# Kernel tuning notes

Measured on AMD Instinct MI355X. Metric: run time of the kernel, lower is better.

Reference implementation:

```python
import jax, jax.numpy as jnp
from jax import lax
import numpy as np

B, H, W = 4, 512, 512
CIN, COUT, BASE, NL = 3, 3, 64, 4
EPS = 1e-5


def _conv(x, w, b, stride=1, pad=0):
    y = lax.conv_general_dilated(x, w, (stride, stride), ((pad, pad), (pad, pad)),
                                 dimension_numbers=('NCHW', 'OIHW', 'NCHW'))
    return y + b[None, :, None, None]


def _convT(x, w, b):
    # torch ConvTranspose2d(k=3, stride=2, padding=1, output_padding=1); w is [Cin, Cout, 3, 3]
    w_ = jnp.flip(w, (2, 3)).transpose(1, 0, 2, 3)  # -> OIHW
    k = w.shape[2]
    lo, hi = k - 1 - 1, k - 1 - 1 + 1  # (1, 2): pad=1, output_padding=1
    y = lax.conv_general_dilated(x, w_, (1, 1), ((lo, hi), (lo, hi)), lhs_dilation=(2, 2),
                                 dimension_numbers=('NCHW', 'OIHW', 'NCHW'))
    return y + b[None, :, None, None]


def _inorm(x):
    m = x.mean((2, 3), keepdims=True)
    v = x.var((2, 3), keepdims=True)  # biased, matches torch InstanceNorm2d
    return (x - m) * lax.rsqrt(v + EPS)


def _refl(x, p=3):
    return jnp.pad(x, ((0, 0), (0, 0), (p, p), (p, p)), mode='reflect')


def setup_inputs() -> dict:
    key = jax.random.key(0)
    ks = jax.random.split(key, 16)
    s = 0.05
    inp = {}
    inp['x'] = jax.random.normal(ks[0], (B, CIN, H, W), jnp.float32)
    inp['inst'] = jax.random.randint(ks[1], (B, 1, H, W), 0, 10)
    inp['w0'] = jax.random.normal(ks[2], (BASE, CIN, 7, 7), jnp.float32) * s
    inp['b0'] = jnp.zeros((BASE,), jnp.float32)
    c, ki = BASE, 3
    for i in range(NL):
        inp[f'dw{i}'] = jax.random.normal(ks[ki], (2 * c, c, 3, 3), jnp.float32) * s
        inp[f'db{i}'] = jnp.zeros((2 * c,), jnp.float32)
        c *= 2; ki += 1
    for i in range(NL):
        inp[f'uw{i}'] = jax.random.normal(ks[ki], (c, c // 2, 3, 3), jnp.float32) * s  # torch ConvT layout [Cin,Cout,k,k]
        inp[f'ub{i}'] = jnp.zeros((c // 2,), jnp.float32)
        c //= 2; ki += 1
    inp['wf'] = jax.random.normal(ks[ki], (COUT, BASE, 7, 7), jnp.float32) * s
    inp['bf'] = jnp.zeros((COUT,), jnp.float32)
    return inp


def reference(x, w0, b0, dw0, db0, dw1, db1, dw2, db2, dw3, db3,
              uw0, ub0, uw1, ub1, uw2, ub2, uw3, ub3, wf, bf, inst):
    h = jax.nn.relu(_inorm(_conv(_refl(x), w0, b0)))
    for w_, b_ in ((dw0, db0), (dw1, db1), (dw2, db2), (dw3, db3)):
        h = jax.nn.relu(_inorm(_conv(h, w_, b_, stride=2, pad=1)))
    for w_, b_ in ((uw0, ub0), (uw1, ub1), (uw2, ub2), (uw3, ub3)):
        h = jax.nn.relu(_inorm(_convT(h, w_, b_)))
    h = jnp.tanh(_conv(_refl(h), wf, bf))
    # instancewise_average_pooling: original loops classes but always masks inst==1,
    # so the result is the per-(batch, channel) mean over inst==1 pixels scattered
    # back onto those pixels, zeros elsewhere.
    mask = (inst == 1).astype(h.dtype)            # [B,1,H,W]
    cnt = mask.sum((2, 3))                        # [B,1]
    mean = (h * mask).sum((2, 3)) / cnt           # [B,C]
    return mean[:, :, None, None] * mask
```

## Files before the change

kernel.cpp:

```cpp
#include <hip/hip_runtime.h>
#include <math.h>


typedef _Float16 half_t;
typedef _Float16 halfx8 __attribute__((ext_vector_type(8)));
typedef _Float16 halfx4 __attribute__((ext_vector_type(4)));
typedef float floatx4 __attribute__((ext_vector_type(4)));

static __device__ __forceinline__ float xform(float v, float m, float r) {
  v = (v - m) * r;
  return v > 0.f ? v : 0.f;
}

__global__ __launch_bounds__(256) void transform_w(
    const float* __restrict__ src, half_t* __restrict__ dst,
    int Cin, int Cout, int mode)
{
  int idx = blockIdx.x * 256 + threadIdx.x;
  int total = Cin * Cout * 9;
  if (idx >= total) return;
  int tap = idx % 9, t2 = idx / 9;
  int co, ci;
  if (mode == 0) { ci = t2 % Cin; co = t2 / Cin; }
  else           { co = t2 % Cout; ci = t2 / Cout; }
  dst[((size_t)tap * Cout + co) * Cin + ci] = (half_t)src[idx];
}

__global__ __launch_bounds__(256) void transform_wf(
    const float* __restrict__ src, half_t* __restrict__ dst)
{
  int idx = blockIdx.x * 256 + threadIdx.x;
  if (idx >= 49 * 16 * 64) return;
  int ci = idx & 63, t = idx >> 6;
  int co = t & 15, tap = t >> 4;
  float v = (co < 3) ? src[((size_t)co * 64 + ci) * 49 + tap] : 0.f;
  dst[idx] = (half_t)v;
}

__global__ __launch_bounds__(256) void conv0_kernel(
    const float* __restrict__ x, const float* __restrict__ w,
    const float* __restrict__ bias, half_t* __restrict__ out)
{
  const int H = 512, W = 512, CIN = 3;
  __shared__ float s_in[3][22][22];
  __shared__ float4 s_w[3 * 49][4];
  const int cog = blockIdx.x, tile = blockIdx.y, b = blockIdx.z;
  const int tx0 = (tile & 31) << 4, ty0 = (tile >> 5) << 4;
  const int tid = threadIdx.x, tx = tid & 15, ty = tid >> 4;

  for (int idx = tid; idx < CIN * 49 * 16; idx += 256) {
    int j = idx & 15, r = idx >> 4;
    ((float*)s_w)[r * 16 + j] = w[(cog * 16 + j) * (CIN * 49) + r];
  }
  for (int idx = tid; idx < CIN * 22 * 22; idx += 256) {
    int ci = idx / 484, rr = idx % 484;
    int iy = rr / 22, ix = rr % 22;
    int gy = ty0 + iy - 3, gx = tx0 + ix - 3;
    gy = gy < 0 ? -gy : (gy >= H ? 2 * H - 2 - gy : gy);
    gx = gx < 0 ? -gx : (gx >= W ? 2 * W - 2 - gx : gx);
    s_in[ci][iy][ix] = x[((size_t)(b * CIN + ci) * H + gy) * W + gx];
  }
  __syncthreads();

  float acc[16];
#pragma unroll
  for (int j = 0; j < 16; ++j) acc[j] = 0.f;

#pragma unroll
  for (int ci = 0; ci < 3; ++ci)
    for (int ky = 0; ky < 7; ++ky)
#pragma unroll
      for (int kx = 0; kx < 7; ++kx) {
        float v = s_in[ci][ty + ky][tx + kx];
        int r = (ci * 7 + ky) * 7 + kx;
#pragma unroll
        for (int q = 0; q < 4; ++q) {
          float4 wv = s_w[r][q];
          acc[q * 4 + 0] += v * wv.x;
          acc[q * 4 + 1] += v * wv.y;
          acc[q * 4 + 2] += v * wv.z;
          acc[q * 4 + 3] += v * wv.w;
        }
      }
  const int oy = ty0 + ty, ox = tx0 + tx;
  halfx8 o0, o1;
#pragma unroll
  for (int j = 0; j < 8; ++j) {
    o0[j] = (half_t)(acc[j] + bias[cog * 16 + j]);
    o1[j] = (half_t)(acc[8 + j] + bias[cog * 16 + 8 + j]);
  }
  size_t obase = ((size_t)(b * 512 + oy) * 512 + ox) * 64 + cog * 16;
  *(halfx8*)(&out[obase]) = o0;
  *(halfx8*)(&out[obase + 8]) = o1;
}

__global__ __launch_bounds__(256) void stats_part(
    const half_t* __restrict__ x, float* __restrict__ Ssum, int C, int S)
{
  const int b = blockIdx.y, tid = threadIdx.x;
  const size_t base = (size_t)b * S * C;
  const int E8 = (S * C) >> 3;
  float s[8], s2[8];
#pragma unroll
  for (int j = 0; j < 8; ++j) { s[j] = 0.f; s2[j] = 0.f; }
  for (int i8 = blockIdx.x * 256 + tid; i8 < E8; i8 += gridDim.x * 256) {
    halfx8 v = *(const halfx8*)(x + base + (size_t)i8 * 8);
#pragma unroll
    for (int j = 0; j < 8; ++j) {
      float f = (float)v[j];
      s[j] += f; s2[j] += f * f;
    }
  }
  __shared__ float part[256][16];
#pragma unroll
  for (int j = 0; j < 8; ++j) { part[tid][j] = s[j]; part[tid][8 + j] = s2[j]; }
  __syncthreads();
  const int T = C >> 3, reps = 256 / (C >> 3);
  for (int c = tid; c < C; c += 256) {
    int r = c >> 3, j = c & 7;
    float ss = 0.f, ss2 = 0.f;
    for (int m = 0; m < reps; ++m) {
      ss += part[r + m * T][j];
      ss2 += part[r + m * T][8 + j];
    }
    atomicAdd(&Ssum[(size_t)(b * C + c) * 2], ss);
    atomicAdd(&Ssum[(size_t)(b * C + c) * 2 + 1], ss2);
  }
}

__global__ __launch_bounds__(256) void finalize_stats(
    const float* __restrict__ Ssum, float* __restrict__ mean,
    float* __restrict__ rstd, int total, float invN)
{
  int idx = blockIdx.x * 256 + threadIdx.x;
  if (idx >= total) return;
  float sm = Ssum[(size_t)idx * 2], s2 = Ssum[(size_t)idx * 2 + 1];
  float m = sm * invN;
  float var = s2 * invN - m * m;
  mean[idx] = m;
  rstd[idx] = rsqrtf(var + 1e-5f);
}

__global__ __launch_bounds__(256) void down_mfma(
    const half_t* __restrict__ in, const half_t* __restrict__ wt,
    const float* __restrict__ bias, const float* __restrict__ mean,
    const float* __restrict__ rstd, half_t* __restrict__ out,
    int Cin, int Cout, int IH, int IW)
{
  const int OH = IH >> 1, OW = IW >> 1;
  __shared__ _Float16 sX[9 * 33 * 40];
  const int tid = threadIdx.x;
  const int wave = tid >> 6, lane = tid & 63;
  const int ln = lane & 15, g = lane >> 4;
  const int cog = blockIdx.x, b = blockIdx.z;
  const int ntx = OW >> 4;
  const int ox0 = (blockIdx.y % ntx) << 4, oy0 = (blockIdx.y / ntx) << 2;
  const int iy0 = 2 * oy0 - 1, ix0 = 2 * ox0 - 1;
  const int coW = cog * 128 + wave * 32;
  const int q = tid & 3;

  floatx4 acc[4][2];
#pragma unroll
  for (int r = 0; r < 4; ++r)
#pragma unroll
    for (int n = 0; n < 2; ++n) acc[r][n] = floatx4{0.f, 0.f, 0.f, 0.f};

  for (int c0 = 0; c0 < Cin; c0 += 32) {
    float mq[8], rq[8];
#pragma unroll
    for (int j = 0; j < 8; ++j) {
      int cc = c0 + q * 8 + j;
      mq[j] = mean[b * Cin + cc];
      rq[j] = rstd[b * Cin + cc];
    }
    __syncthreads();
    for (int idx = tid; idx < 9 * 33 * 4; idx += 256) {
      int p = idx >> 2;
      int y = p / 33, xx = p % 33;
      int gy = iy0 + y, gx = ix0 + xx;
      halfx8 v = {0, 0, 0, 0, 0, 0, 0, 0};
      if ((unsigned)gy < (unsigned)IH && (unsigned)gx < (unsigned)IW) {
        v = *(const halfx8*)(in + ((size_t)(b * IH + gy) * IW + gx) * Cin + c0 + q * 8);
#pragma unroll
        for (int j = 0; j < 8; ++j) {
          float f = ((float)v[j] - mq[j]) * rq[j];
          v[j] = (_Float16)(f > 0.f ? f : 0.f);
        }
      }
      *(halfx8*)(&sX[(y * 33 + xx) * 40 + q * 8]) = v;
    }
    __syncthreads();
#pragma unroll
    for (int tap = 0; tap < 9; ++tap) {
      const int ky = tap / 3, kx = tap % 3;
      halfx8 wb0 = *(const halfx8*)(wt + ((size_t)tap * Cout + coW + ln) * Cin + c0 + g * 8);
      halfx8 wb1 = *(const halfx8*)(wt + ((size_t)tap * Cout + coW + 16 + ln) * Cin + c0 + g * 8);
#pragma unroll
      for (int r = 0; r < 4; ++r) {
        halfx8 a = *(const halfx8*)(&sX[((2 * r + ky) * 33 + 2 * ln + kx) * 40 + g * 8]);
        acc[r][0] = __builtin_amdgcn_mfma_f32_16x16x32_f16(a, wb0, acc[r][0], 0, 0, 0);
        acc[r][1] = __builtin_amdgcn_mfma_f32_16x16x32_f16(a, wb1, acc[r][1], 0, 0, 0);
      }
    }
  }
#pragma unroll
  for (int nt = 0; nt < 2; ++nt) {
    int co = coW + nt * 16 + ln;
    float bs = bias[co];
#pragma unroll
    for (int r = 0; r < 4; ++r)
#pragma unroll
      for (int i = 0; i < 4; ++i) {
        int oy = oy0 + r, ox = ox0 + g * 4 + i;
        out[((size_t)(b * OH + oy) * OW + ox) * Cout + co] = (half_t)(acc[r][nt][i] + bs);
      }
  }
}

__global__ __launch_bounds__(256) void up_mfma(
    const half_t* __restrict__ in, const half_t* __restrict__ wt,
    const float* __restrict__ bias, const float* __restrict__ mean,
    const float* __restrict__ rstd, half_t* __restrict__ out,
    int Cin, int Cout, int IH, int IW)
{
  const int OH = IH << 1, OW = IW << 1;
  __shared__ _Float16 sX[5 * 17 * 40];
  const int tid = threadIdx.x;
  const int wave = tid >> 6, lane = tid & 63;
  const int ln = lane & 15, g = lane >> 4;
  const int cog = blockIdx.x, b = blockIdx.z;
  const int ntx = OW >> 5;
  const int ox0 = (blockIdx.y % ntx) << 5, oy0 = (blockIdx.y / ntx) << 3;
  const int iyb = oy0 >> 1, ixb = ox0 >> 1;
  const int co = cog * 64 + wave * 16 + ln;
  const int q = tid & 3;

  floatx4 acc[4][4];
#pragma unroll
  for (int c = 0; c < 4; ++c)
#pragma unroll
    for (int r = 0; r < 4; ++r) acc[c][r] = floatx4{0.f, 0.f, 0.f, 0.f};

  for (int c0 = 0; c0 < Cin; c0 += 32) {
    float mq[8], rq[8];
#pragma unroll
    for (int j = 0; j < 8; ++j) {
      int cc = c0 + q * 8 + j;
      mq[j] = mean[b * Cin + cc];
      rq[j] = rstd[b * Cin + cc];
    }
    __syncthreads();
    for (int idx = tid; idx < 5 * 17 * 4; idx += 256) {
      int p = idx >> 2;
      int y = p / 17, xx = p % 17;
      int gy = iyb + y, gx = ixb + xx;
      halfx8 v = {0, 0, 0, 0, 0, 0, 0, 0};
      if (gy < IH && gx < IW) {
        v = *(const halfx8*)(in + ((size_t)(b * IH + gy) * IW + gx) * Cin + c0 + q * 8);
#pragma unroll
        for (int j = 0; j < 8; ++j) {
          float f = ((float)v[j] - mq[j]) * rq[j];
          v[j] = (_Float16)(f > 0.f ? f : 0.f);
        }
      }
      *(halfx8*)(&sX[(y * 17 + xx) * 40 + q * 8]) = v;
    }
    __syncthreads();
#pragma unroll
    for (int tap = 0; tap < 9; ++tap) {
      const int ky = tap / 3, kx = tap % 3;
      const int cls = ((ky == 1) ? 0 : 2) + ((kx == 1) ? 0 : 1);
      const int dy = (ky == 0) ? 1 : 0;
      const int dx = (kx == 0) ? 1 : 0;
      halfx8 wb = *(const halfx8*)(wt + ((size_t)tap * Cout + co) * Cin + c0 + g * 8);
#pragma unroll
      for (int r = 0; r < 4; ++r) {
        halfx8 a = *(const halfx8*)(&sX[((r + dy) * 17 + ln + dx) * 40 + g * 8]);
        acc[cls][r] = __builtin_amdgcn_mfma_f32_16x16x32_f16(a, wb, acc[cls][r], 0, 0, 0);
      }
    }
  }
  float bs = bias[co];
#pragma unroll
  for (int cls = 0; cls < 4; ++cls) {
    const int ey = cls >> 1, ex = cls & 1;
#pragma unroll
    for (int r = 0; r < 4; ++r)
#pragma unroll
      for (int i = 0; i < 4; ++i) {
        int oy = oy0 + 2 * r + ey;
        int ox = ox0 + 2 * (g * 4 + i) + ex;
        out[((size_t)(b * OH + oy) * OW + ox) * Cout + co] = (half_t)(acc[cls][r][i] + bs);
      }
  }
}

__global__ __launch_bounds__(256) void convf_mfma(
    const half_t* __restrict__ in, const half_t* __restrict__ wt,
    const float* __restrict__ bias, const float* __restrict__ mean,
    const float* __restrict__ rstd, float* __restrict__ out)
{
  const int H = 512, W = 512;
  __shared__ _Float16 sX[22 * 22 * 72];
  const int tile = blockIdx.x, b = blockIdx.y;
  const int tx0 = (tile & 31) << 4, ty0 = (tile >> 5) << 4;
  const int tid = threadIdx.x;
  const int wave = tid >> 6, lane = tid & 63;
  const int ln = lane & 15, g = lane >> 4;
  const int oct = tid & 7;

  float mq[8], rq[8];
#pragma unroll
  for (int j = 0; j < 8; ++j) {
    mq[j] = mean[b * 64 + oct * 8 + j];
    rq[j] = rstd[b * 64 + oct * 8 + j];
  }
  for (int u = tid; u < 484 * 8; u += 256) {
    int p = u >> 3;
    int iy = p / 22, ix = p % 22;
    int gy = ty0 + iy - 3, gx = tx0 + ix - 3;
    gy = gy < 0 ? -gy : (gy >= H ? 2 * H - 2 - gy : gy);
    gx = gx < 0 ? -gx : (gx >= W ? 2 * W - 2 - gx : gx);
    halfx8 v = *(const halfx8*)(in + ((size_t)(b * H + gy) * W + gx) * 64 + oct * 8);
#pragma unroll
    for (int j = 0; j < 8; ++j) {
      float f = ((float)v[j] - mq[j]) * rq[j];
      v[j] = (_Float16)(f > 0.f ? f : 0.f);
    }
    *(halfx8*)(&sX[p * 72 + oct * 8]) = v;
  }
  __syncthreads();

  floatx4 acc[4];
#pragma unroll
  for (int r = 0; r < 4; ++r) acc[r] = floatx4{0.f, 0.f, 0.f, 0.f};

  for (int tap = 0; tap < 49; ++tap) {
    const int ky = tap / 7, kx = tap % 7;
#pragma unroll
    for (int kc = 0; kc < 2; ++kc) {
      halfx8 wb = *(const halfx8*)(wt + ((size_t)tap * 16 + ln) * 64 + kc * 32 + g * 8);
#pragma unroll
      for (int rr = 0; rr < 4; ++rr) {
        int y = wave * 4 + rr;
        halfx8 a = *(const halfx8*)(&sX[((y + ky) * 22 + ln + kx) * 72 + kc * 32 + g * 8]);
        acc[rr] = __builtin_amdgcn_mfma_f32_16x16x32_f16(a, wb, acc[rr], 0, 0, 0);
      }
    }
  }
  if (ln < 3) {
    float bs = bias[ln];
#pragma unroll
    for (int rr = 0; rr < 4; ++rr) {
      int oy = ty0 + wave * 4 + rr;
#pragma unroll
      for (int i = 0; i < 4; ++i) {
        int ox = tx0 + g * 4 + i;
        out[((size_t)(b * 3 + ln) * H + oy) * W + ox] = tanhf(acc[rr][i] + bs);
      }
    }
  }
}

__global__ __launch_bounds__(256) void pool_sum_kernel(
    const float* __restrict__ f, const int* __restrict__ inst,
    float* __restrict__ P)
{
  const int N = 512 * 512;
  const int b = blockIdx.x, chunk = blockIdx.y;
  const int per = N / 32;
  const int base = chunk * per;
  float s0 = 0.f, s1 = 0.f, s2 = 0.f, c = 0.f;
  for (int i = base + threadIdx.x; i < base + per; i += 256) {
    if (inst[b * N + i] == 1) {
      c += 1.f;
      s0 += f[(size_t)(b * 3 + 0) * N + i];
      s1 += f[(size_t)(b * 3 + 1) * N + i];
      s2 += f[(size_t)(b * 3 + 2) * N + i];
    }
  }
#pragma unroll
  for (int off = 32; off > 0; off >>= 1) {
    s0 += __shfl_down(s0, off); s1 += __shfl_down(s1, off);
    s2 += __shfl_down(s2, off); c += __shfl_down(c, off);
  }
  __shared__ float red[4][4];
  int wv = threadIdx.x >> 6;
  if ((threadIdx.x & 63) == 0) {
    red[wv][0] = s0; red[wv][1] = s1; red[wv][2] = s2; red[wv][3] = c;
  }
  __syncthreads();
  if (threadIdx.x == 0) {
    float t0 = red[0][0] + red[1][0] + red[2][0] + red[3][0];
    float t1 = red[0][1] + red[1][1] + red[2][1] + red[3][1];
    float t2 = red[0][2] + red[1][2] + red[2][2] + red[3][2];
    float tc = red[0][3] + red[1][3] + red[2][3] + red[3][3];
    atomicAdd(&P[b * 4 + 0], t0);
    atomicAdd(&P[b * 4 + 1], t1);
    atomicAdd(&P[b * 4 + 2], t2);
    atomicAdd(&P[b * 4 + 3], tc);
  }
}

__global__ __launch_bounds__(256) void pool_scatter_kernel(
    const int* __restrict__ inst, const float* __restrict__ P,
    float* __restrict__ out)
{
  const int N = 512 * 512;
  int idx = blockIdx.x * 256 + threadIdx.x;
  if (idx >= 4 * N) return;
  int b = idx >> 18;
  int i = idx & (N - 1);
  bool m = inst[idx] == 1;
  float inv = 1.f / P[b * 4 + 3];
  out[(size_t)(b * 3 + 0) * N + i] = m ? P[b * 4 + 0] * inv : 0.f;
  out[(size_t)(b * 3 + 1) * N + i] = m ? P[b * 4 + 1] * inv : 0.f;
  out[(size_t)(b * 3 + 2) * N + i] = m ? P[b * 4 + 2] * inv : 0.f;
}

extern "C" void kernel_launch(void* const* d_in, const int* in_sizes, int n_in,
                              void* d_out, int out_size, void* d_ws, size_t ws_size,
                              hipStream_t stream)
{
  (void)in_sizes; (void)n_in; (void)out_size; (void)ws_size;
  const float* x    = (const float*)d_in[0];
  const int*   inst = (const int*)d_in[1];
  const float* w0   = (const float*)d_in[2];
  const float* b0   = (const float*)d_in[3];
  const float *dw[4], *db[4], *uw[4], *ub[4];
  for (int i = 0; i < 4; ++i) {
    dw[i] = (const float*)d_in[4 + 2 * i];
    db[i] = (const float*)d_in[5 + 2 * i];
    uw[i] = (const float*)d_in[12 + 2 * i];
    ub[i] = (const float*)d_in[13 + 2 * i];
  }
  const float* wf = (const float*)d_in[20];
  const float* bf = (const float*)d_in[21];

  char* base = (char*)d_ws;
  half_t* A  = (half_t*)base;
  half_t* Bh = (half_t*)(base + 134217728);
  float*  F  = (float*)(base + 134217728);
  float*  Ssum   = (float*)(base + 201326592);
  float*  S_mean = (float*)(base + 201326592 + 32768);
  float*  S_rstd = (float*)(base + 201326592 + 49152);
  float*  P      = (float*)(base + 201326592 + 65536);
  half_t* WTp0   = (half_t*)(base + 201326592 + 66560);
  half_t* WTp1   = (half_t*)(base + 201326592 + 66560 + 147456);
  half_t* WTf    = (half_t*)(base + 201326592 + 66560 + 294912);
  half_t* WTA    = (half_t*)(base + 124780544);
  half_t* WTB    = (half_t*)(base + 191889408);

  auto XFORM = [&](const float* src, half_t* dst, int Ci, int Co, int mode) {
    int tot = Ci * Co * 9;
    transform_w<<<dim3((tot + 255) / 256), 256, 0, stream>>>(src, dst, Ci, Co, mode);
  };
  auto STATS = [&](const half_t* p, int C, int S) {
    hipMemsetAsync(Ssum, 0, 4096 * 2 * sizeof(float), stream);
    stats_part<<<dim3(128, 4), 256, 0, stream>>>(p, Ssum, C, S);
    finalize_stats<<<dim3((4 * C + 255) / 256), 256, 0, stream>>>(
        Ssum, S_mean, S_rstd, 4 * C, 1.f / (float)S);
  };

  conv0_kernel<<<dim3(4, 1024, 4), 256, 0, stream>>>(x, w0, b0, A);
  transform_wf<<<dim3((49 * 16 * 64 + 255) / 256), 256, 0, stream>>>(wf, WTf);
  STATS(A, 64, 512 * 512);

  XFORM(dw[0], WTp0, 64, 128, 0);
  down_mfma<<<dim3(1, 1024, 4), 256, 0, stream>>>(A, WTp0, db[0], S_mean, S_rstd, Bh, 64, 128, 512, 512);
  STATS(Bh, 128, 256 * 256);
  XFORM(dw[1], WTA, 128, 256, 0);
  down_mfma<<<dim3(2, 256, 4), 256, 0, stream>>>(Bh, WTA, db[1], S_mean, S_rstd, A, 128, 256, 256, 256);
  STATS(A, 256, 128 * 128);
  XFORM(dw[2], WTB, 256, 512, 0);
  down_mfma<<<dim3(4, 64, 4), 256, 0, stream>>>(A, WTB, db[2], S_mean, S_rstd, Bh, 256, 512, 128, 128);
  STATS(Bh, 512, 64 * 64);
  XFORM(dw[3], WTA, 512, 1024, 0);
  down_mfma<<<dim3(8, 16, 4), 256, 0, stream>>>(Bh, WTA, db[3], S_mean, S_rstd, A, 512, 1024, 64, 64);
  STATS(A, 1024, 32 * 32);

  XFORM(uw[0], WTB, 1024, 512, 1);
  up_mfma<<<dim3(8, 16, 4), 256, 0, stream>>>(A, WTB, ub[0], S_mean, S_rstd, Bh, 1024, 512, 32, 32);
  STATS(Bh, 512, 64 * 64);
  XFORM(uw[1], WTA, 512, 256, 1);
  up_mfma<<<dim3(4, 64, 4), 256, 0, stream>>>(Bh, WTA, ub[1], S_mean, S_rstd, A, 512, 256, 64, 64);
  STATS(A, 256, 128 * 128);
  XFORM(uw[2], WTA, 256, 128, 1);
  up_mfma<<<dim3(2, 256, 4), 256, 0, stream>>>(A, WTA, ub[2], S_mean, S_rstd, Bh, 256, 128, 128, 128);
  STATS(Bh, 128, 256 * 256);
  XFORM(uw[3], WTp1, 128, 64, 1);
  up_mfma<<<dim3(1, 1024, 4), 256, 0, stream>>>(Bh, WTp1, ub[3], S_mean, S_rstd, A, 128, 64, 256, 256);
  STATS(A, 64, 512 * 512);

  convf_mfma<<<dim3(1024, 4), 256, 0, stream>>>(A, WTf, bf, S_mean, S_rstd, F);
  hipMemsetAsync(P, 0, 16 * sizeof(float), stream);
  pool_sum_kernel<<<dim3(4, 32), 256, 0, stream>>>(F, inst, P);
  pool_scatter_kernel<<<dim3(4096), 256, 0, stream>>>(inst, P, (float*)d_out);
}
```

Baseline: 1.856 ms.

## Rewrite 7x7 stem convolution as fp16 MFMA implicit GEMM

```diff
diff --git a/kernel.cpp b/kernel.cpp
--- a/kernel.cpp
+++ b/kernel.cpp
@@ -37,61 +37,90 @@
   dst[idx] = (half_t)v;
 }
 
-__global__ __launch_bounds__(256) void conv0_kernel(
-    const float* __restrict__ x, const float* __restrict__ w,
+__global__ __launch_bounds__(256) void transform_w0(
+    const float* __restrict__ src, half_t* __restrict__ dst)
+{
+  int idx = blockIdx.x * 256 + threadIdx.x;
+  if (idx >= 7 * 64 * 32) return;
+  int k = idx & 31, t = idx >> 5;
+  int co = t & 63, ky = t >> 6;
+  int kx = k >> 2, ci = k & 3;
+  float v = (ci < 3 && kx < 7) ? src[(((size_t)co * 3 + ci) * 7 + ky) * 7 + kx] : 0.f;
+  dst[idx] = (half_t)v;
+}
+
+__global__ __launch_bounds__(256) void conv0_mfma(
+    const float* __restrict__ x, const half_t* __restrict__ wt,
     const float* __restrict__ bias, half_t* __restrict__ out)
 {
-  const int H = 512, W = 512, CIN = 3;
-  __shared__ float s_in[3][22][22];
-  __shared__ float4 s_w[3 * 49][4];
-  const int cog = blockIdx.x, tile = blockIdx.y, b = blockIdx.z;
+  const int H = 512, W = 512;
+  __shared__ _Float16 sX[22 * 24 * 4];
+  __shared__ _Float16 sO[256 * 72];
+  const int tile = blockIdx.x, b = blockIdx.y;
   const int tx0 = (tile & 31) << 4, ty0 = (tile >> 5) << 4;
-  const int tid = threadIdx.x, tx = tid & 15, ty = tid >> 4;
-
-  for (int idx = tid; idx < CIN * 49 * 16; idx += 256) {
-    int j = idx & 15, r = idx >> 4;
-    ((float*)s_w)[r * 16 + j] = w[(cog * 16 + j) * (CIN * 49) + r];
-  }
-  for (int idx = tid; idx < CIN * 22 * 22; idx += 256) {
-    int ci = idx / 484, rr = idx % 484;
-    int iy = rr / 22, ix = rr % 22;
-    int gy = ty0 + iy - 3, gx = tx0 + ix - 3;
-    gy = gy < 0 ? -gy : (gy >= H ? 2 * H - 2 - gy : gy);
-    gx = gx < 0 ? -gx : (gx >= W ? 2 * W - 2 - gx : gx);
-    s_in[ci][iy][ix] = x[((size_t)(b * CIN + ci) * H + gy) * W + gx];
+  const int tid = threadIdx.x;
+  const int wave = tid >> 6, lane = tid & 63;
+  const int ln = lane & 15, g = lane >> 4;
+
+  for (int u = tid; u < 22 * 24; u += 256) {
+    int row = u / 24, col = u % 24;
+    halfx4 v = {0, 0, 0, 0};
+    if (col < 22) {
+      int gy = ty0 + row - 3, gx = tx0 + col - 3;
+      gy = gy < 0 ? -gy : (gy >= H ? 2 * H - 2 - gy : gy);
+      gx = gx < 0 ? -gx : (gx >= W ? 2 * W - 2 - gx : gx);
+      size_t p = (size_t)b * 3 * H * W + (size_t)gy * W + gx;
+      v[0] = (_Float16)x[p];
+      v[1] = (_Float16)x[p + H * W];
+      v[2] = (_Float16)x[p + 2 * H * W];
+    }
+    *(halfx4*)(&sX[u * 4]) = v;
   }
   __syncthreads();
 
-  float acc[16];
-#pragma unroll
-  for (int j = 0; j < 16; ++j) acc[j] = 0.f;
-
-#pragma unroll
-  for (int ci = 0; ci < 3; ++ci)
-    for (int ky = 0; ky < 7; ++ky)
-#pragma unroll
-      for (int kx = 0; kx < 7; ++kx) {
-        float v = s_in[ci][ty + ky][tx + kx];
-        int r = (ci * 7 + ky) * 7 + kx;
-#pragma unroll
-        for (int q = 0; q < 4; ++q) {
-          float4 wv = s_w[r][q];
-          acc[q * 4 + 0] += v * wv.x;
-          acc[q * 4 + 1] += v * wv.y;
-          acc[q * 4 + 2] += v * wv.z;
-          acc[q * 4 + 3] += v * wv.w;
-        }
-      }
-  const int oy = ty0 + ty, ox = tx0 + tx;
-  halfx8 o0, o1;
-#pragma unroll
-  for (int j = 0; j < 8; ++j) {
-    o0[j] = (half_t)(acc[j] + bias[cog * 16 + j]);
-    o1[j] = (half_t)(acc[8 + j] + bias[cog * 16 + 8 + j]);
-  }
-  size_t obase = ((size_t)(b * 512 + oy) * 512 + ox) * 64 + cog * 16;
-  *(halfx8*)(&out[obase]) = o0;
-  *(halfx8*)(&out[obase + 8]) = o1;
+  floatx4 acc[4][4];
+#pragma unroll
+  for (int r = 0; r < 4; ++r)
+#pragma unroll
+    for (int n = 0; n < 4; ++n) acc[r][n] = floatx4{0.f, 0.f, 0.f, 0.f};
+
+#pragma unroll
+  for (int ky = 0; ky < 7; ++ky) {
+    halfx8 wb[4];
+#pragma unroll
+    for (int nt = 0; nt < 4; ++nt)
+      wb[nt] = *(const halfx8*)(wt + ((size_t)ky * 64 + nt * 16 + ln) * 32 + g * 8);
+#pragma unroll
+    for (int rr = 0; rr < 4; ++rr) {
+      int y = wave * 4 + rr;
+      halfx8 a = *(const halfx8*)(&sX[((y + ky) * 24 + ln + 2 * g) * 4]);
+#pragma unroll
+      for (int nt = 0; nt < 4; ++nt)
+        acc[rr][nt] = __builtin_amdgcn_mfma_f32_16x16x32_f16(a, wb[nt], acc[rr][nt], 0, 0, 0);
+    }
+  }
+
+  float bs[4];
+#pragma unroll
+  for (int nt = 0; nt < 4; ++nt) bs[nt] = bias[nt * 16 + ln];
+#pragma unroll
+  for (int rr = 0; rr < 4; ++rr)
+#pragma unroll
+    for (int nt = 0; nt < 4; ++nt)
+#pragma unroll
+      for (int i = 0; i < 4; ++i) {
+        int p = (wave * 4 + rr) * 16 + g * 4 + i;
+        sO[p * 72 + nt * 16 + ln] = (half_t)(acc[rr][nt][i] + bs[nt]);
+      }
+  __syncthreads();
+  {
+    int p = tid;
+    int oy = ty0 + (p >> 4), ox = tx0 + (p & 15);
+    size_t ob = ((size_t)(b * 512 + oy) * 512 + ox) * 64;
+#pragma unroll
+    for (int j = 0; j < 8; ++j)
+      *(halfx8*)(&out[ob + j * 8]) = *(const halfx8*)(&sO[p * 72 + j * 8]);
+  }
 }
 
 __global__ __launch_bounds__(256) void stats_part(
@@ -448,6 +477,7 @@
   half_t* WTp0   = (half_t*)(base + 201326592 + 66560);
   half_t* WTp1   = (half_t*)(base + 201326592 + 66560 + 147456);
   half_t* WTf    = (half_t*)(base + 201326592 + 66560 + 294912);
+  half_t* WT0    = (half_t*)(base + 201326592 + 66560 + 294912 + 100352);
   half_t* WTA    = (half_t*)(base + 124780544);
   half_t* WTB    = (half_t*)(base + 191889408);
 
@@ -462,8 +492,9 @@
         Ssum, S_mean, S_rstd, 4 * C, 1.f / (float)S);
   };
 
-  conv0_kernel<<<dim3(4, 1024, 4), 256, 0, stream>>>(x, w0, b0, A);
+  transform_w0<<<dim3((7 * 64 * 32 + 255) / 256), 256, 0, stream>>>(w0, WT0);
   transform_wf<<<dim3((49 * 16 * 64 + 255) / 256), 256, 0, stream>>>(wf, WTf);
+  conv0_mfma<<<dim3(1024, 4), 256, 0, stream>>>(x, WT0, b0, A);
   STATS(A, 64, 512 * 512);
 
   XFORM(dw[0], WTp0, 64, 128, 0);
```

New measurement: 1.591 ms. 1.17x faster.
